# Performance work log

Measured on AMD Instinct MI355X. Metric: run time of the kernel, lower is better.

## Reference

```python
import jax, jax.numpy as jnp
import numpy as np

EMBED_DIM = 256
B, H, S = 8, 20, 1024


def setup_inputs() -> dict:
    key = jax.random.key(0)
    ks = jax.random.split(key, 10)
    E = EMBED_DIM
    d2, d4 = 2 * E, 4 * E

    def lin(kw, kb, out_dim, in_dim):
        bound = 1.0 / np.sqrt(in_dim)
        w = jax.random.uniform(kw, (out_dim, in_dim), minval=-bound, maxval=bound, dtype=jnp.float32)
        b = jax.random.uniform(kb, (out_dim,), minval=-bound, maxval=bound, dtype=jnp.float32)
        return w, b

    wc_w, wc_b = lin(ks[0], ks[1], d2, d2)
    wh_w, wh_b = lin(ks[2], ks[3], d2, d2)
    qt_w, qt_b = lin(ks[4], ks[5], 1, d2)
    wf_w, wf_b = lin(ks[6], ks[7], E, d4)

    hist = jax.random.normal(ks[8], (B, H, S, d2), dtype=jnp.float32)
    cur = jax.random.normal(ks[9], (B, S, d2), dtype=jnp.float32)
    return {
        "wca_history_embeddings": hist,
        "wca_current_embeddings": cur,
        "wc_w": wc_w, "wc_b": wc_b,
        "wh_w": wh_w, "wh_b": wh_b,
        "qt_w": qt_w, "qt_b": qt_b,
        "wf_w": wf_w, "wf_b": wf_b,
    }


def reference(wca_history_embeddings, wca_current_embeddings,
              wc_w, wc_b, wh_w, wh_b, qt_w, qt_b, wf_w, wf_b):
    # hist: [B, H, S, 2E]; cur: [B, S, 2E]
    c_proj = jnp.einsum('bsd,ed->bse', wca_current_embeddings, wc_w) + wc_b   # [B,S,2E]
    h_proj = jnp.einsum('bhsd,ed->bhse', wca_history_embeddings, wh_w) + wh_b  # [B,H,S,2E]
    gate = jax.nn.sigmoid(c_proj[:, None, :, :] + h_proj)                      # [B,H,S,2E]
    # alpha[b,h,s] = qt(gate) -- raw scores, NO softmax (matches original)
    alpha = jnp.einsum('bhse,e->bhs', gate, qt_w[0]) + qt_b[0]                 # [B,H,S]
    # weighted neighbor sum over history dim
    summed = jnp.einsum('bhs,bhsd->bsd', alpha, wca_history_embeddings)        # [B,S,2E]
    fused = jnp.concatenate([wca_current_embeddings, summed], axis=-1)         # [B,S,4E]
    final = jnp.einsum('bsd,ed->bse', fused, wf_w) + wf_b                      # [B,S,E]
    return final
```

## Files before the change

### kernel.cpp

```cpp
#include <hip/hip_runtime.h>
#include <hip/hip_bf16.h>
#include <stdint.h>

static constexpr int Bn = 8, Hn = 20, Sn = 1024, En = 256, D2 = 512, D4 = 1024;
static constexpr int Mall = Bn * Hn * Sn;
static constexpr int BS   = Bn * Sn;

typedef __attribute__((ext_vector_type(8))) short bf16x8;
typedef __attribute__((ext_vector_type(4))) float f32x4;

__device__ __forceinline__ unsigned short f2bf(float f) {
  unsigned int u = __float_as_uint(f);
  u += 0x7FFFu + ((u >> 16) & 1u);
  return (unsigned short)(u >> 16);
}
__device__ __forceinline__ float bf2f(unsigned short u) {
  return __uint_as_float(((unsigned int)u) << 16);
}
__device__ __forceinline__ float sigmoid_fast(float x) {
  return __builtin_amdgcn_rcpf(1.0f + __expf(-x));
}
__device__ __forceinline__ unsigned int packbf_trunc(float a, float b) {
  return __builtin_amdgcn_perm(__float_as_uint(b), __float_as_uint(a),
                               0x07060302u);
}
__device__ __forceinline__ uint4 pack8_trunc(float4 f0, float4 f1) {
  uint4 p;
  p.x = packbf_trunc(f0.x, f0.y);
  p.y = packbf_trunc(f0.z, f0.w);
  p.z = packbf_trunc(f1.x, f1.y);
  p.w = packbf_trunc(f1.z, f1.w);
  return p;
}
__device__ __forceinline__ bf16x8 pack2(float4 f0, float4 f1) {
  union { uint4 u; bf16x8 b; } c;
  c.u = pack8_trunc(f0, f1);
  return c.b;
}

typedef const __attribute__((address_space(1))) void gv_t;
typedef __attribute__((address_space(3))) void lv_t;
__device__ __forceinline__ void gload_lds16(const void* g, void* l) {
  __builtin_amdgcn_global_load_lds((gv_t*)g, (lv_t*)l, 16, 0, 0);
}

__global__ __launch_bounds__(256) void k_convert_weights(
    const float* __restrict__ wc, const float* __restrict__ wh,
    const float* __restrict__ wf,
    unsigned short* __restrict__ wcb, unsigned short* __restrict__ whb,
    unsigned short* __restrict__ wfb) {
  int idx4 = blockIdx.x * 256 + threadIdx.x;
  int a = idx4 >> 16;
  int r = idx4 & 65535;
  const float* s = (a == 0) ? wc : (a == 1) ? wh : wf;
  unsigned short* d = (a == 0) ? wcb : (a == 1) ? whb : wfb;
  float4 v = reinterpret_cast<const float4*>(s)[r];
  ushort4 o;
  o.x = f2bf(v.x); o.y = f2bf(v.y); o.z = f2bf(v.z); o.w = f2bf(v.w);
  reinterpret_cast<ushort4*>(d)[r] = o;
}

template <int MODE>
__global__ __launch_bounds__(256) void k_gemm_bt(
    const float* __restrict__ A,
    const unsigned short* __restrict__ Bw,
    const float* __restrict__ bias,
    const unsigned short* __restrict__ cproj,
    const float* __restrict__ qtw,
    const float* __restrict__ qtb,
    unsigned short* __restrict__ cproj_out,
    float* __restrict__ alpha_out) {
  __shared__ __align__(16) unsigned char ldsA[128 * 128];
  __shared__ __align__(16) unsigned char ldsB[128 * 128];

  const int tid = threadIdx.x;
  const int lane = tid & 63, wave = tid >> 6;
  const int lrow = lane & 15, lk = lane >> 4;
  const int row0 = blockIdx.x * 128;
  const f32x4 zero4 = {0.f, 0.f, 0.f, 0.f};

  float asum[2][4];
  if (MODE == 1) {
#pragma unroll
    for (int rf = 0; rf < 2; ++rf)
#pragma unroll
      for (int r = 0; r < 4; ++r) asum[rf][r] = 0.f;
  }

  const int nc_begin = (MODE == 0) ? blockIdx.y : 0;
  const int nc_end   = (MODE == 0) ? (int)blockIdx.y + 1 : 4;

  for (int nc = nc_begin; nc < nc_end; ++nc) {
    f32x4 acc[2][8];
#pragma unroll
    for (int rf = 0; rf < 2; ++rf)
#pragma unroll
      for (int cf = 0; cf < 8; ++cf) acc[rf][cf] = zero4;

    for (int kt = 0; kt < 8; ++kt) {
      __syncthreads();
#pragma unroll
      for (int slot = 0; slot < 4; ++slot) {
        int idx = (slot * 256 + tid) * 8;
        int row = idx >> 6, k = idx & 63;
        const float* src = A + (size_t)(row0 + row) * 512 + kt * 64 + k;
        float4 f0 = *reinterpret_cast<const float4*>(src);
        float4 f1 = *reinterpret_cast<const float4*>(src + 4);
        uint4 p = pack8_trunc(f0, f1);
        int off = row * 128 + ((k * 2) ^ ((row & 7) << 4));
        *reinterpret_cast<uint4*>(ldsA + off) = p;
      }
#pragma unroll
      for (int c = 0; c < 4; ++c) {
        int ci = c * 256 + tid;
        int n = ci >> 3, kc = (ci & 7) * 8;
        const unsigned short* src =
            Bw + (size_t)(nc * 128 + n) * 512 + kt * 64 + kc;
        uint4 p = *reinterpret_cast<const uint4*>(src);
        int off = n * 128 + ((kc * 2) ^ ((n & 7) << 4));
        *reinterpret_cast<uint4*>(ldsB + off) = p;
      }
      __syncthreads();
#pragma unroll
      for (int ks = 0; ks < 2; ++ks) {
        int kbyte = ks * 64 + lk * 16;
        bf16x8 af[2];
#pragma unroll
        for (int rf = 0; rf < 2; ++rf) {
          int ar = wave * 32 + rf * 16 + lrow;
          af[rf] = *reinterpret_cast<const bf16x8*>(
              ldsA + ar * 128 + (kbyte ^ ((ar & 7) << 4)));
        }
#pragma unroll
        for (int cf = 0; cf < 8; ++cf) {
          int br = cf * 16 + lrow;
          bf16x8 bf = *reinterpret_cast<const bf16x8*>(
              ldsB + br * 128 + (kbyte ^ ((br & 7) << 4)));
#pragma unroll
          for (int rf = 0; rf < 2; ++rf)
            acc[rf][cf] = __builtin_amdgcn_mfma_f32_16x16x32_bf16(
                af[rf], bf, acc[rf][cf], 0, 0, 0);
        }
      }
    }

    if (MODE == 0) {
#pragma unroll
      for (int cf = 0; cf < 8; ++cf) {
        int e = nc * 128 + cf * 16 + lrow;
        float bse = bias[e];
#pragma unroll
        for (int rf = 0; rf < 2; ++rf)
#pragma unroll
          for (int r = 0; r < 4; ++r) {
            int row = row0 + wave * 32 + rf * 16 + lk * 4 + r;
            cproj_out[(size_t)row * 512 + e] = f2bf(acc[rf][cf][r] + bse);
          }
      }
    } else {
#pragma unroll
      for (int cf = 0; cf < 8; ++cf) {
        int e = nc * 128 + cf * 16 + lrow;
        float whb = bias[e];
        float qw = qtw[e];
#pragma unroll
        for (int rf = 0; rf < 2; ++rf)
#pragma unroll
          for (int r = 0; r < 4; ++r) {
            int row = row0 + wave * 32 + rf * 16 + lk * 4 + r;
            int bsrow = ((row / (Hn * Sn)) << 10) | (row & 1023);
            float cp = bf2f(cproj[(size_t)bsrow * 512 + e]);
            float g = sigmoid_fast(acc[rf][cf][r] + whb + cp);
            asum[rf][r] = fmaf(g, qw, asum[rf][r]);
          }
      }
    }
  }

  if (MODE == 1) {
#pragma unroll
    for (int off = 1; off < 16; off <<= 1) {
#pragma unroll
      for (int rf = 0; rf < 2; ++rf)
#pragma unroll
        for (int r = 0; r < 4; ++r)
          asum[rf][r] += __shfl_xor(asum[rf][r], off, 64);
    }
    if (lrow == 0) {
      float qb = qtb[0];
#pragma unroll
      for (int rf = 0; rf < 2; ++rf)
#pragma unroll
        for (int r = 0; r < 4; ++r) {
          int row = row0 + wave * 32 + rf * 16 + lk * 4 + r;
          alpha_out[row] = asum[rf][r] + qb;
        }
    }
  }
}

__global__ __launch_bounds__(256, 2) void k_alpha(
    const float* __restrict__ A,
    const unsigned short* __restrict__ Bw,
    const float* __restrict__ bias,
    const unsigned short* __restrict__ cproj,
    const float* __restrict__ qtw,
    const float* __restrict__ qtb,
    float* __restrict__ alpha) {
  __shared__ __align__(16) unsigned char ldsA[16384];
  __shared__ __align__(16) unsigned char ldsB[65536];

  const int tid = threadIdx.x;
  const int lane = tid & 63, wave = tid >> 6;
  const int lrow = lane & 15, lk = lane >> 4;
  const int wr = wave >> 1, wc = wave & 1;
  const int row0 = blockIdx.x * 64;
  const f32x4 zero4 = {0.f, 0.f, 0.f, 0.f};

  const int arow = tid >> 4;
  const int aslot = (tid & 15) ^ (arow & 15);
  const float* gA0 = A + (size_t)(row0 + arow) * 512 + aslot * 4;
  const int brow = tid >> 3;
  const int bslot = (tid & 7) ^ (brow & 7);
  const unsigned short* gB0 = Bw + (size_t)brow * 512 + bslot * 8;
  char* lA = (char*)ldsA + wave * 1024;
  char* lB = (char*)ldsB + wave * 1024;

  f32x4 acc[2][16];
#pragma unroll
  for (int m = 0; m < 2; ++m)
#pragma unroll
    for (int n = 0; n < 16; ++n) acc[m][n] = zero4;

  for (int kt = 0; kt < 8; ++kt) {
    __syncthreads();
#pragma unroll
    for (int j = 0; j < 4; ++j)
      gload_lds16(gA0 + j * 8192 + kt * 64, lA + j * 4096);
#pragma unroll
    for (int j = 0; j < 16; ++j)
      gload_lds16(gB0 + j * 16384 + kt * 64, lB + j * 4096);
    __syncthreads();
#pragma unroll
    for (int ks = 0; ks < 2; ++ks) {
      bf16x8 af[2];
#pragma unroll
      for (int m = 0; m < 2; ++m) {
        int r = wr * 32 + m * 16 + lrow;
        int q0 = (ks * 8 + lk * 2) ^ (r & 15);
        int q1 = (ks * 8 + lk * 2 + 1) ^ (r & 15);
        float4 d0 = *reinterpret_cast<const float4*>(ldsA + r * 256 + q0 * 16);
        float4 d1 = *reinterpret_cast<const float4*>(ldsA + r * 256 + q1 * 16);
        af[m] = pack2(d0, d1);
      }
#pragma unroll
      for (int n = 0; n < 16; ++n) {
        int r = wc * 256 + n * 16 + lrow;
        int slot = (ks * 4 + lk) ^ (r & 7);
        bf16x8 bfr = *reinterpret_cast<const bf16x8*>(ldsB + r * 128 + slot * 16);
#pragma unroll
        for (int m = 0; m < 2; ++m)
          acc[m][n] = __builtin_amdgcn_mfma_f32_16x16x32_bf16(af[m], bfr,
                                                              acc[m][n], 0, 0, 0);
      }
    }
  }

  float asum[2][4];
#pragma unroll
  for (int m = 0; m < 2; ++m)
#pragma unroll
    for (int r = 0; r < 4; ++r) asum[m][r] = 0.f;

  const int bs_base = (row0 / (Hn * Sn)) * 1024 + (row0 & 1023);
#pragma unroll
  for (int n = 0; n < 16; ++n) {
    int e = wc * 256 + n * 16 + lrow;
    float whb = bias[e];
    float qw = qtw[e];
#pragma unroll
    for (int m = 0; m < 2; ++m)
#pragma unroll
      for (int r = 0; r < 4; ++r) {
        int t = wr * 32 + m * 16 + lk * 4 + r;
        float cp = bf2f(cproj[(size_t)(bs_base + t) * 512 + e]);
        float g = sigmoid_fast(acc[m][n][r] + whb + cp);
        asum[m][r] = fmaf(g, qw, asum[m][r]);
      }
  }

#pragma unroll
  for (int off = 1; off < 16; off <<= 1) {
#pragma unroll
    for (int m = 0; m < 2; ++m)
#pragma unroll
      for (int r = 0; r < 4; ++r)
        asum[m][r] += __shfl_xor(asum[m][r], off, 64);
  }

  __syncthreads();
  float* red = reinterpret_cast<float*>(ldsA);
  if (lrow == 0) {
#pragma unroll
    for (int m = 0; m < 2; ++m)
#pragma unroll
      for (int r = 0; r < 4; ++r) {
        int t = wr * 32 + m * 16 + lk * 4 + r;
        red[wc * 64 + t] = asum[m][r];
      }
  }
  __syncthreads();
  if (tid < 64) alpha[row0 + tid] = red[tid] + red[64 + tid] + qtb[0];
}

__global__ __launch_bounds__(256) void k_summed(
    const float* __restrict__ hist, const float* __restrict__ alpha,
    unsigned short* __restrict__ summed) {
  int idx = blockIdx.x * 256 + threadIdx.x;
  int bs = idx >> 7, c4 = idx & 127;
  int b = bs >> 10, s = bs & 1023;
  const float4* hp = reinterpret_cast<const float4*>(hist);
  float4 acc = make_float4(0.f, 0.f, 0.f, 0.f);
#pragma unroll
  for (int h = 0; h < Hn; ++h) {
    int bh = b * Hn + h;
    float a = alpha[(bh << 10) + s];
    float4 v = hp[(size_t)(bh * 1024 + s) * 128 + c4];
    acc.x = fmaf(a, v.x, acc.x);
    acc.y = fmaf(a, v.y, acc.y);
    acc.z = fmaf(a, v.z, acc.z);
    acc.w = fmaf(a, v.w, acc.w);
  }
  ushort4 o;
  o.x = f2bf(acc.x); o.y = f2bf(acc.y); o.z = f2bf(acc.z); o.w = f2bf(acc.w);
  reinterpret_cast<ushort4*>(summed)[idx] = o;
}

__global__ __launch_bounds__(256) void k_final(
    const float* __restrict__ cur,
    const unsigned short* __restrict__ summed,
    const unsigned short* __restrict__ wfb16,
    const float* __restrict__ wf_bias,
    float* __restrict__ out) {
  __shared__ __align__(16) unsigned char ldsA[64 * 128];
  __shared__ __align__(16) unsigned char ldsB[128 * 128];
  const int tid = threadIdx.x;
  const int lane = tid & 63, wave = tid >> 6;
  const int lrow = lane & 15, lk = lane >> 4;
  const int row0 = blockIdx.x * 64;
  const int n0 = blockIdx.y * 128;
  const f32x4 zero4 = {0.f, 0.f, 0.f, 0.f};

  f32x4 acc[8];
#pragma unroll
  for (int cf = 0; cf < 8; ++cf) acc[cf] = zero4;

  for (int kt = 0; kt < 16; ++kt) {
    __syncthreads();
#pragma unroll
    for (int slot = 0; slot < 2; ++slot) {
      int idx = (slot * 256 + tid) * 8;
      int row = idx >> 6, k = idx & 63;
      int gcol = kt * 64 + k;
      uint4 p;
      if (kt < 8) {
        const float* src = cur + (size_t)(row0 + row) * 512 + gcol;
        float4 f0 = *reinterpret_cast<const float4*>(src);
        float4 f1 = *reinterpret_cast<const float4*>(src + 4);
        p = pack8_trunc(f0, f1);
      } else {
        p = *reinterpret_cast<const uint4*>(
            summed + (size_t)(row0 + row) * 512 + gcol - 512);
      }
      int off = row * 128 + ((k * 2) ^ ((row & 7) << 4));
      *reinterpret_cast<uint4*>(ldsA + off) = p;
    }
#pragma unroll
    for (int c = 0; c < 4; ++c) {
      int ci = c * 256 + tid;
      int n = ci >> 3, kc = (ci & 7) * 8;
      uint4 p = *reinterpret_cast<const uint4*>(
          wfb16 + (size_t)(n0 + n) * 1024 + kt * 64 + kc);
      int off = n * 128 + ((kc * 2) ^ ((n & 7) << 4));
      *reinterpret_cast<uint4*>(ldsB + off) = p;
    }
    __syncthreads();
#pragma unroll
    for (int ks = 0; ks < 2; ++ks) {
      int kbyte = ks * 64 + lk * 16;
      int ar = wave * 16 + lrow;
      bf16x8 a = *reinterpret_cast<const bf16x8*>(
          ldsA + ar * 128 + (kbyte ^ ((ar & 7) << 4)));
#pragma unroll
      for (int cf = 0; cf < 8; ++cf) {
        int br = cf * 16 + lrow;
        bf16x8 b = *reinterpret_cast<const bf16x8*>(
            ldsB + br * 128 + (kbyte ^ ((br & 7) << 4)));
        acc[cf] = __builtin_amdgcn_mfma_f32_16x16x32_bf16(a, b, acc[cf], 0, 0, 0);
      }
    }
  }
#pragma unroll
  for (int cf = 0; cf < 8; ++cf) {
    int col = n0 + cf * 16 + lrow;
    float bse = wf_bias[col];
#pragma unroll
    for (int r = 0; r < 4; ++r) {
      int row = row0 + wave * 16 + lk * 4 + r;
      out[(size_t)row * 256 + col] = acc[cf][r] + bse;
    }
  }
}

extern "C" void kernel_launch(void* const* d_in, const int* in_sizes, int n_in,
                              void* d_out, int out_size, void* d_ws,
                              size_t ws_size, hipStream_t stream) {
  (void)in_sizes; (void)n_in; (void)out_size;
  const float* hist = (const float*)d_in[0];
  const float* cur  = (const float*)d_in[1];
  const float* wc_w = (const float*)d_in[2];
  const float* wc_b = (const float*)d_in[3];
  const float* wh_w = (const float*)d_in[4];
  const float* wh_b = (const float*)d_in[5];
  const float* qt_w = (const float*)d_in[6];
  const float* qt_b = (const float*)d_in[7];
  const float* wf_w = (const float*)d_in[8];
  const float* wf_b = (const float*)d_in[9];
  float* out = (float*)d_out;
  char* ws = (char*)d_ws;

  unsigned short* wcb    = (unsigned short*)(ws);
  unsigned short* whb    = (unsigned short*)(ws + 524288);
  unsigned short* wfb    = (unsigned short*)(ws + 1048576);
  unsigned short* cproj  = (unsigned short*)(ws + 1572864);
  float*          alpha  = (float*)(ws + 9961472);
  unsigned short* summed = (unsigned short*)(ws + 10616832);
  const size_t NEED = 19005440;

  k_convert_weights<<<dim3(768), dim3(256), 0, stream>>>(wc_w, wh_w, wf_w, wcb,
                                                         whb, wfb);
  k_gemm_bt<0><<<dim3(BS / 128, 4), dim3(256), 0, stream>>>(
      cur, wcb, wc_b, nullptr, nullptr, nullptr, cproj, nullptr);
  if (ws_size >= NEED) {
    k_alpha<<<dim3(Mall / 64), dim3(256), 0, stream>>>(hist, whb, wh_b, cproj,
                                                       qt_w, qt_b, alpha);
  } else {
    k_gemm_bt<1><<<dim3(Mall / 128, 1), dim3(256), 0, stream>>>(
        hist, whb, wh_b, cproj, qt_w, qt_b, nullptr, alpha);
  }
  k_summed<<<dim3(4096), dim3(256), 0, stream>>>(hist, alpha, summed);
  k_final<<<dim3(BS / 64, 2), dim3(256), 0, stream>>>(cur, summed, wfb, wf_b,
                                                      out);
}
```

Baseline: 246.9 us.

## Fuse alpha scoring and history weighted sum into one kernel keeping hist in LDS

Each block now covers all 20 history rows for 4 sequence positions, converts the full hist tile to bf16 in LDS, and reuses that tile both for the projection GEMM and the alpha-weighted sum over history. This removes the separate k_summed pass that re-read the whole fp32 history tensor and the alpha round trip through global memory. The A loads are software-pipelined through registers two K-steps ahead. The costs are a large LDS footprint (about 150 KB) limiting occupancy to one block per CU, and the weighted sum now uses bf16-rounded history instead of fp32.

```diff
diff --git a/kernel.cpp b/kernel.cpp
--- a/kernel.cpp
+++ b/kernel.cpp
@@ -23,6 +23,9 @@
 __device__ __forceinline__ unsigned int packbf_trunc(float a, float b) {
   return __builtin_amdgcn_perm(__float_as_uint(b), __float_as_uint(a),
                                0x07060302u);
+}
+__device__ __forceinline__ unsigned int packbf_rne(float a, float b) {
+  return ((unsigned int)f2bf(b) << 16) | (unsigned int)f2bf(a);
 }
 __device__ __forceinline__ uint4 pack8_trunc(float4 f0, float4 f1) {
   uint4 p;
@@ -31,11 +34,6 @@
   p.z = packbf_trunc(f1.x, f1.y);
   p.w = packbf_trunc(f1.z, f1.w);
   return p;
-}
-__device__ __forceinline__ bf16x8 pack2(float4 f0, float4 f1) {
-  union { uint4 u; bf16x8 b; } c;
-  c.u = pack8_trunc(f0, f1);
-  return c.b;
 }
 
 typedef const __attribute__((address_space(1))) void gv_t;
@@ -199,118 +197,173 @@
   }
 }
 
-__global__ __launch_bounds__(256, 2) void k_alpha(
+__global__ __launch_bounds__(256, 1) void k_alpha_summed(
     const float* __restrict__ A,
     const unsigned short* __restrict__ Bw,
     const float* __restrict__ bias,
     const unsigned short* __restrict__ cproj,
     const float* __restrict__ qtw,
     const float* __restrict__ qtb,
-    float* __restrict__ alpha) {
-  __shared__ __align__(16) unsigned char ldsA[16384];
+    unsigned short* __restrict__ summed) {
+  __shared__ __align__(16) unsigned char ldsA[81920];
   __shared__ __align__(16) unsigned char ldsB[65536];
+  __shared__ __align__(16) unsigned char ldsC[4096];
 
   const int tid = threadIdx.x;
   const int lane = tid & 63, wave = tid >> 6;
   const int lrow = lane & 15, lk = lane >> 4;
-  const int wr = wave >> 1, wc = wave & 1;
-  const int row0 = blockIdx.x * 64;
+  const int wc = wave;
+  const int b = blockIdx.x >> 8;
+  const int s0 = (blockIdx.x & 255) * 4;
+  const size_t rowbase = (size_t)b * 20480;
   const f32x4 zero4 = {0.f, 0.f, 0.f, 0.f};
 
-  const int arow = tid >> 4;
-  const int aslot = (tid & 15) ^ (arow & 15);
-  const float* gA0 = A + (size_t)(row0 + arow) * 512 + aslot * 4;
+  float4 pa[5];
+  auto issueA = [&](int sl) {
+#pragma unroll
+    for (int j = 0; j < 5; ++j) {
+      int f = j * 256 + tid;
+      int mr = f >> 4, q = f & 15;
+      pa[j] = *reinterpret_cast<const float4*>(
+          A + (rowbase + (size_t)(mr >> 2) * 1024 + s0 + (mr & 3)) * 512 +
+          sl * 64 + q * 4);
+    }
+  };
+  auto writeA = [&](int sl) {
+#pragma unroll
+    for (int j = 0; j < 5; ++j) {
+      int f = j * 256 + tid;
+      int mr = f >> 4, q = f & 15;
+      unsigned int u0 = packbf_rne(pa[j].x, pa[j].y);
+      unsigned int u1 = packbf_rne(pa[j].z, pa[j].w);
+      int g = sl * 8 + (q >> 1);
+      int off = mr * 1024 + ((g ^ (mr & 7)) << 4) + ((q & 1) << 3);
+      *reinterpret_cast<uint2*>(ldsA + off) = make_uint2(u0, u1);
+    }
+  };
+
   const int brow = tid >> 3;
   const int bslot = (tid & 7) ^ (brow & 7);
   const unsigned short* gB0 = Bw + (size_t)brow * 512 + bslot * 8;
-  char* lA = (char*)ldsA + wave * 1024;
   char* lB = (char*)ldsB + wave * 1024;
 
-  f32x4 acc[2][16];
-#pragma unroll
-  for (int m = 0; m < 2; ++m)
-#pragma unroll
-    for (int n = 0; n < 16; ++n) acc[m][n] = zero4;
+  {
+    const unsigned short* csrc = cproj + ((size_t)b * 1024 + s0) * 512;
+    gload_lds16(csrc + tid * 8, (char*)ldsC + wave * 1024);
+  }
+  issueA(0); writeA(0);
+  issueA(1); writeA(1);
+
+  f32x4 acc[5][8];
+#pragma unroll
+  for (int tm = 0; tm < 5; ++tm)
+#pragma unroll
+    for (int n = 0; n < 8; ++n) acc[tm][n] = zero4;
 
   for (int kt = 0; kt < 8; ++kt) {
     __syncthreads();
 #pragma unroll
-    for (int j = 0; j < 4; ++j)
-      gload_lds16(gA0 + j * 8192 + kt * 64, lA + j * 4096);
-#pragma unroll
     for (int j = 0; j < 16; ++j)
       gload_lds16(gB0 + j * 16384 + kt * 64, lB + j * 4096);
-    __syncthreads();
+    __builtin_amdgcn_sched_barrier(0);
+    if (kt < 6) {
+      issueA(kt + 2);
+      __builtin_amdgcn_sched_barrier(0);
+      asm volatile("s_waitcnt vmcnt(5)" ::: "memory");
+    } else {
+      asm volatile("s_waitcnt vmcnt(0)" ::: "memory");
+    }
+    __builtin_amdgcn_s_barrier();
+    __builtin_amdgcn_sched_barrier(0);
 #pragma unroll
     for (int ks = 0; ks < 2; ++ks) {
-      bf16x8 af[2];
-#pragma unroll
-      for (int m = 0; m < 2; ++m) {
-        int r = wr * 32 + m * 16 + lrow;
-        int q0 = (ks * 8 + lk * 2) ^ (r & 15);
-        int q1 = (ks * 8 + lk * 2 + 1) ^ (r & 15);
-        float4 d0 = *reinterpret_cast<const float4*>(ldsA + r * 256 + q0 * 16);
-        float4 d1 = *reinterpret_cast<const float4*>(ldsA + r * 256 + q1 * 16);
-        af[m] = pack2(d0, d1);
-      }
-#pragma unroll
-      for (int n = 0; n < 16; ++n) {
-        int r = wc * 256 + n * 16 + lrow;
+      bf16x8 af[5];
+#pragma unroll
+      for (int tm = 0; tm < 5; ++tm) {
+        int r = tm * 16 + lrow;
+        int g = (kt * 8 + ks * 4 + lk) ^ (r & 7);
+        af[tm] = *reinterpret_cast<const bf16x8*>(ldsA + r * 1024 + g * 16);
+      }
+#pragma unroll
+      for (int n = 0; n < 8; ++n) {
+        int r = wc * 128 + n * 16 + lrow;
         int slot = (ks * 4 + lk) ^ (r & 7);
-        bf16x8 bfr = *reinterpret_cast<const bf16x8*>(ldsB + r * 128 + slot * 16);
-#pragma unroll
-        for (int m = 0; m < 2; ++m)
-          acc[m][n] = __builtin_amdgcn_mfma_f32_16x16x32_bf16(af[m], bfr,
-                                                              acc[m][n], 0, 0, 0);
-      }
-    }
-  }
-
-  float asum[2][4];
-#pragma unroll
-  for (int m = 0; m < 2; ++m)
-#pragma unroll
-    for (int r = 0; r < 4; ++r) asum[m][r] = 0.f;
-
-  const int bs_base = (row0 / (Hn * Sn)) * 1024 + (row0 & 1023);
-#pragma unroll
-  for (int n = 0; n < 16; ++n) {
-    int e = wc * 256 + n * 16 + lrow;
+        bf16x8 bv =
+            *reinterpret_cast<const bf16x8*>(ldsB + r * 128 + slot * 16);
+#pragma unroll
+        for (int tm = 0; tm < 5; ++tm)
+          acc[tm][n] = __builtin_amdgcn_mfma_f32_16x16x32_bf16(af[tm], bv,
+                                                               acc[tm][n], 0,
+                                                               0, 0);
+      }
+    }
+    if (kt < 6) writeA(kt + 2);
+  }
+
+  float asum[5][4];
+#pragma unroll
+  for (int tm = 0; tm < 5; ++tm)
+#pragma unroll
+    for (int r = 0; r < 4; ++r) asum[tm][r] = 0.f;
+
+  const unsigned short* cpl = reinterpret_cast<const unsigned short*>(ldsC);
+#pragma unroll
+  for (int n = 0; n < 8; ++n) {
+    int e = wc * 128 + n * 16 + lrow;
     float whb = bias[e];
     float qw = qtw[e];
-#pragma unroll
-    for (int m = 0; m < 2; ++m)
+    float cpv[4];
+#pragma unroll
+    for (int si = 0; si < 4; ++si) cpv[si] = bf2f(cpl[si * 512 + e]);
+#pragma unroll
+    for (int tm = 0; tm < 5; ++tm)
 #pragma unroll
       for (int r = 0; r < 4; ++r) {
-        int t = wr * 32 + m * 16 + lk * 4 + r;
-        float cp = bf2f(cproj[(size_t)(bs_base + t) * 512 + e]);
-        float g = sigmoid_fast(acc[m][n][r] + whb + cp);
-        asum[m][r] = fmaf(g, qw, asum[m][r]);
-      }
-  }
-
-#pragma unroll
-  for (int off = 1; off < 16; off <<= 1) {
-#pragma unroll
-    for (int m = 0; m < 2; ++m)
+        float g = sigmoid_fast(acc[tm][n][r] + whb + cpv[r]);
+        asum[tm][r] = fmaf(g, qw, asum[tm][r]);
+      }
+  }
+#pragma unroll
+  for (int off = 1; off < 16; off <<= 1)
+#pragma unroll
+    for (int tm = 0; tm < 5; ++tm)
 #pragma unroll
       for (int r = 0; r < 4; ++r)
-        asum[m][r] += __shfl_xor(asum[m][r], off, 64);
-  }
+        asum[tm][r] += __shfl_xor(asum[tm][r], off, 64);
 
   __syncthreads();
-  float* red = reinterpret_cast<float*>(ldsA);
+  float* red = reinterpret_cast<float*>(ldsC);
   if (lrow == 0) {
 #pragma unroll
-    for (int m = 0; m < 2; ++m)
-#pragma unroll
-      for (int r = 0; r < 4; ++r) {
-        int t = wr * 32 + m * 16 + lk * 4 + r;
-        red[wc * 64 + t] = asum[m][r];
-      }
+    for (int tm = 0; tm < 5; ++tm)
+#pragma unroll
+      for (int r = 0; r < 4; ++r)
+        red[wc * 80 + tm * 16 + lk * 4 + r] = asum[tm][r];
   }
   __syncthreads();
-  if (tid < 64) alpha[row0 + tid] = red[tid] + red[64 + tid] + qtb[0];
+
+  const int si = wave;
+  const float qb = qtb[0];
+  float o[8];
+#pragma unroll
+  for (int j = 0; j < 8; ++j) o[j] = 0.f;
+#pragma unroll
+  for (int h = 0; h < 20; ++h) {
+    int mr = h * 4 + si;
+    float a = red[mr] + red[80 + mr] + red[160 + mr] + red[240 + mr] + qb;
+    int g = lane ^ (mr & 7);
+    bf16x8 av = *reinterpret_cast<const bf16x8*>(ldsA + mr * 1024 + g * 16);
+#pragma unroll
+    for (int j = 0; j < 8; ++j)
+      o[j] = fmaf(a, bf2f((unsigned short)av[j]), o[j]);
+  }
+  uint4 pk;
+  pk.x = packbf_rne(o[0], o[1]);
+  pk.y = packbf_rne(o[2], o[3]);
+  pk.z = packbf_rne(o[4], o[5]);
+  pk.w = packbf_rne(o[6], o[7]);
+  size_t orow = (size_t)b * 1024 + s0 + si;
+  reinterpret_cast<uint4*>(summed)[orow * 64 + lane] = pk;
 }
 
 __global__ __launch_bounds__(256) void k_summed(
@@ -442,13 +495,13 @@
   k_gemm_bt<0><<<dim3(BS / 128, 4), dim3(256), 0, stream>>>(
       cur, wcb, wc_b, nullptr, nullptr, nullptr, cproj, nullptr);
   if (ws_size >= NEED) {
-    k_alpha<<<dim3(Mall / 64), dim3(256), 0, stream>>>(hist, whb, wh_b, cproj,
-                                                       qt_w, qt_b, alpha);
+    k_alpha_summed<<<dim3(2048), dim3(256), 0, stream>>>(
+        hist, whb, wh_b, cproj, qt_w, qt_b, summed);
   } else {
     k_gemm_bt<1><<<dim3(Mall / 128, 1), dim3(256), 0, stream>>>(
         hist, whb, wh_b, cproj, qt_w, qt_b, nullptr, alpha);
-  }
-  k_summed<<<dim3(4096), dim3(256), 0, stream>>>(hist, alpha, summed);
+    k_summed<<<dim3(4096), dim3(256), 0, stream>>>(hist, alpha, summed);
+  }
   k_final<<<dim3(BS / 64, 2), dim3(256), 0, stream>>>(cur, summed, wfb, wf_b,
                                                       out);
 }
```

New measurement: 273.2 us. +10.7%, slower.
